# Kernel tuning notes

Hardware: AMD Instinct MI355X
Metric: run time of the kernel (lower is better)

The kernel has to match this reference:

```python
import jax, jax.numpy as jnp
import numpy as np

K1, K2, K3 = 36, 36, 2  # rolled-patch sizes hardcoded in unfolding()


def _patch_indices(C, H, W, k1=K1, k2=K2, k3=K3):
    """Precompute gather indices replacing the triple-nested torch.roll loops.

    Column col=(k*k2+j)*k1+i of Ak_3D holds X rolled by (k,i,j) along (C,H,W):
      A[b, c*H*W+h*W+w, col] = X[b, (c-k)%C, (h-i)%H, (w-j)%W]
    The adjoint gathers with +k,+i,+j shifts.
    """
    Kc = k1 * k2 * k3
    col = np.arange(Kc)
    kk = col // (k1 * k2)
    jj = (col % (k1 * k2)) // k1
    ii = col % k1
    cg, hg, wg = np.meshgrid(np.arange(C), np.arange(H), np.arange(W), indexing='ij')
    cg = cg.reshape(-1, 1); hg = hg.reshape(-1, 1); wg = wg.reshape(-1, 1)
    fwd = ((cg - kk) % C) * (H * W) + ((hg - ii) % H) * W + ((wg - jj) % W)
    adj = ((cg + kk) % C) * (H * W) + ((hg + ii) % H) * W + ((wg + jj) % W)
    return jnp.asarray(fwd, jnp.int32), jnp.asarray(adj, jnp.int32)


def _unfold(input_img, S0, alpha, beta, gamma, iters):
    B, C, H, W = input_img.shape
    m = C * H * W
    mk = (H * W) // 64
    Kc = K1 * K2 * K3
    fwd_idx, adj_idx = _patch_indices(C, H, W)
    colr = jnp.arange(Kc, dtype=jnp.int32)

    def Ak(x):  # [B,C,H,W] -> [B, m, Kc] (single gather == Ak_3D)
        return x.reshape(B, m)[:, fwd_idx]

    def Ak_adj(A):  # [B, m, Kc] -> [B,C,H,W] (== Ak_adj_3D)
        g = A[:, adj_idx, colr[None, :]]  # [B, m, Kc]
        return (g.sum(-1) / Kc).reshape(B, C, H, W)

    a3 = alpha[:, None, None]
    g3 = gamma[:, None, None]
    g4 = gamma[:, None, None, None]
    b4 = beta[:, None, None, None]
    I_mk = jnp.eye(mk, dtype=input_img.dtype)

    # t == 0 initialization (L detached, S random-clamped from setup, M/N rect. identities)
    L0 = jax.lax.stop_gradient(input_img)
    M0 = jnp.broadcast_to(jnp.eye(m, mk, dtype=input_img.dtype), (B, m, mk))
    N0 = jnp.broadcast_to(jnp.eye(mk, Kc, dtype=input_img.dtype), (B, mk, Kc))

    def step(carry, _):
        Lc, Sc, Mc, Nc = carry
        MN = Mc @ Nc                                        # [B, m, Kc]
        Ln = jnp.clip((input_img - Sc + g4 * Ak_adj(MN)) / (g4 + 1.0), 0.0, 1.0)
        Sn = (input_img - Ln) / (b4 + 1.0)
        AkL = Ak(Ln)                                        # [B, m, Kc]
        # M-update: 2g * Ak_L N^T pinv(a I + 2g N N^T)
        Cm = a3 * I_mk + 2.0 * g3 * (Nc @ Nc.transpose(0, 2, 1))      # [B, mk, mk]
        Mn = 2.0 * g3 * ((AkL @ Nc.transpose(0, 2, 1)) @ jnp.linalg.pinv(Cm))
        # N-update: 2g * pinv(a I + 2g M^T M) M^T Ak_L
        Cn = a3 * I_mk + 2.0 * g3 * (Mn.transpose(0, 2, 1) @ Mn)      # [B, mk, mk]
        Nn = 2.0 * g3 * (jnp.linalg.pinv(Cn) @ (Mn.transpose(0, 2, 1) @ AkL))
        return (Ln, Sn, Mn, Nn), None

    (Lf, _, _, _), _ = jax.lax.scan(step, (L0, S0, M0, N0), None, length=iters - 1)
    return Lf


def setup_inputs() -> dict:
    key = jax.random.key(0)
    k1, k2 = jax.random.split(key)
    B, C, H, W = 1, 2, 64, 64
    input_img = jax.random.uniform(k1, (B, C, H, W), jnp.float32)
    S0 = jnp.clip(jax.random.normal(k2, (B, C, H, W), jnp.float32), 0.0, 1.0)  # clamp(randn_like,0,1)
    alpha = jnp.full((B,), 10.0, jnp.float32)  # w_alpha
    beta = jnp.full((B,), 2.0, jnp.float32)    # w_beta
    gamma = jnp.full((B,), 10.0, jnp.float32)  # w_gamma
    return {"input_img": input_img, "S0": S0, "alpha": alpha, "beta": beta,
            "gamma": gamma, "iters": 6}


def reference(input_img, S0, alpha, beta, gamma, iters):
    return _unfold(input_img, S0, alpha, beta, gamma, iters)
```

## Files before the change

kernel.cpp:

```cpp
#include <hip/hip_runtime.h>

#define KC 2592
#define KCP 2624
#define HW 4096

#define OFF_L    0u
#define OFF_S    8192u
#define OFF_MT   16384u
#define OFF_NTT  540672u
#define OFF_BIG  708608u
#define OFF_GRAM 2805760u
#define OFF_CMI  2809856u
#define OFF_CNI  2813952u

__global__ __launch_bounds__(256) void k_init(const float* __restrict__ inp, const float* __restrict__ s0,
                                              float* __restrict__ L, float* __restrict__ S,
                                              float* __restrict__ Mt, float* __restrict__ NtT){
  int t = blockIdx.x * 256 + threadIdx.x;
  if (t < 8192){ L[t] = inp[t]; S[t] = s0[t]; }
  if (t < 524288){ int r = t >> 13; int p = t & 8191; Mt[t] = (p == r) ? 1.0f : 0.0f; }
  if (t < 167936){ int r = t / KCP; int d = t - r * KCP;
                   int dr = (r % 36) * 36 + r / 36;
                   NtT[t] = (d == dr) ? 1.0f : 0.0f; }
}

__device__ __forceinline__ float readlane_f(float x, int lane){
  return __uint_as_float(__builtin_amdgcn_readlane(__float_as_uint(x), lane));
}
template<int K>
__device__ __forceinline__ void gj_step(float (&b)[64], int lane){
  float bk = b[K];
  float akk = readlane_f(bk, K);
  float p = 1.0f / akk;
  bool isk = (lane == K);
  float t = isk ? 1.0f : bk;
  float pt = p * t;
  #pragma unroll
  for (int i = 0; i < 64; i++){
    if (i == K) continue;
    float f = readlane_f(b[i], K);
    float base = isk ? 0.0f : b[i];
    b[i] = fmaf(-f, pt, base);
  }
  b[K] = t * p;
}
template<int K> struct GJ {
  static __device__ __forceinline__ void run(float (&b)[64], int lane){
    gj_step<K>(b, lane);
    GJ<K + 1>::run(b, lane);
  }
};
template<> struct GJ<64> {
  static __device__ __forceinline__ void run(float (&b)[64], int lane){}
};
__device__ void inv64(const float* __restrict__ src, const float* __restrict__ pg,
                      const float* __restrict__ pa, float* __restrict__ dst, int lane){
  float scale = 2.0f * pg[0];
  float ad = pa[0];
  float b[64];
  #pragma unroll
  for (int i = 0; i < 64; i++)
    b[i] = scale * src[i * 64 + lane] + ((i == lane) ? ad : 0.0f);
  GJ<0>::run(b, lane);
  #pragma unroll
  for (int i = 0; i < 64; i++)
    dst[i * 64 + lane] = b[i];
}

__global__ __launch_bounds__(128) void k_conv_R(const float* __restrict__ Mtg,
                                                const float* __restrict__ NtT,
                                                float* __restrict__ Rpart){
  __shared__ float img[2][24][68];
  __shared__ float4 filt4[162];
  int r = blockIdx.x, oct = blockIdx.y, z = blockIdx.z, tid = threadIdx.x;
  int rowbase = oct * 16 + z * 9;
  const float4* gi4 = (const float4*)(Mtg + (size_t)r * 8192);
  for (int t = tid; t < 768; t += 128){
    int fw = t & 15, rr = t >> 4;
    int c = (rr >= 24) ? 1 : 0, q = rr - c * 24;
    int gr = (rowbase + q) & 63;
    float4 v4 = gi4[(c * 64 + gr) * 16 + fw];
    float* d = &img[c][q][fw * 4];
    d[0] = v4.x; d[1] = v4.y; d[2] = v4.z; d[3] = v4.w;
  }
  int iilo = z * 9;
  const float* gf = NtT + (size_t)r * KCP;
  for (int t = tid; t < 162; t += 128){
    int kk = t / 81; int rem4 = t - kk * 81;
    filt4[t] = *(const float4*)(gf + kk * 1296 + iilo * 36 + rem4 * 4);
  }
  __syncthreads();
  int c0 = tid >> 6, hl = (tid >> 2) & 15, w0 = (tid & 3) * 16;
  float acc[16];
  #pragma unroll
  for (int u = 0; u < 16; u++) acc[u] = 0.0f;
  #pragma unroll 1
  for (int kk = 0; kk < 2; kk++){
    int cimg = (c0 + kk) & 1;
    #pragma unroll 1
    for (int iix = 0; iix < 9; iix++){
      const float* ib = img[cimg][hl + iix];
      float v[32];
      #pragma unroll
      for (int t = 0; t < 8; t++){
        float4 t4 = *(const float4*)&ib[(w0 + 4 * t) & 63];
        v[4*t] = t4.x; v[4*t+1] = t4.y; v[4*t+2] = t4.z; v[4*t+3] = t4.w;
      }
      const float4* fb = &filt4[kk * 81 + iix * 9];
      #pragma unroll
      for (int g = 0; g < 9; g++){
        float4 ff = fb[g];
        #pragma unroll
        for (int u = 0; u < 16; u++) acc[u] = fmaf(ff.x, v[(4*g + 0 + u) & 31], acc[u]);
        #pragma unroll
        for (int u = 0; u < 16; u++) acc[u] = fmaf(ff.y, v[(4*g + 1 + u) & 31], acc[u]);
        #pragma unroll
        for (int u = 0; u < 16; u++) acc[u] = fmaf(ff.z, v[(4*g + 2 + u) & 31], acc[u]);
        #pragma unroll
        for (int u = 0; u < 16; u++) acc[u] = fmaf(ff.w, v[(4*g + 3 + u) & 31], acc[u]);
        if (g < 5){
          float4 nv = *(const float4*)&ib[(w0 + 32 + 4*g) & 63];
          int s = (4*g) & 31;
          v[s] = nv.x; v[s+1] = nv.y; v[s+2] = nv.z; v[s+3] = nv.w;
        }
      }
    }
  }
  int h = oct * 16 + hl;
  size_t ob = ((size_t)r + 64 * z) * 8192 + (size_t)(c0 * HW + h * 64 + w0);
  *(float4*)&Rpart[ob]      = make_float4(acc[0], acc[1], acc[2], acc[3]);
  *(float4*)&Rpart[ob + 4]  = make_float4(acc[4], acc[5], acc[6], acc[7]);
  *(float4*)&Rpart[ob + 8]  = make_float4(acc[8], acc[9], acc[10], acc[11]);
  *(float4*)&Rpart[ob + 12] = make_float4(acc[12], acc[13], acc[14], acc[15]);
}

__global__ __launch_bounds__(128) void k_conv_T1(const float* __restrict__ Lg,
                                                 const float* __restrict__ NtT,
                                                 float* __restrict__ T1t,
                                                 const float* __restrict__ Gr,
                                                 const float* __restrict__ pg,
                                                 const float* __restrict__ pa,
                                                 float* __restrict__ CmI){
  __shared__ float img[2][24][68];
  __shared__ float4 filt4[162];
  if (blockIdx.z == 4){
    if (blockIdx.x == 0 && blockIdx.y == 0 && threadIdx.x < 64)
      inv64(Gr, pg, pa, CmI, threadIdx.x);
    return;
  }
  int r = blockIdx.x, oct = blockIdx.y, z = blockIdx.z, tid = threadIdx.x;
  int rowbase = (oct * 16 - z * 9 - 8 + 128) & 63;
  const float4* gi4 = (const float4*)Lg;
  for (int t = tid; t < 768; t += 128){
    int fw = t & 15, rr = t >> 4;
    int c = (rr >= 24) ? 1 : 0, q = rr - c * 24;
    int gr = (rowbase + q) & 63;
    float4 v4 = gi4[(c * 64 + gr) * 16 + fw];
    float* d = &img[c][q][fw * 4];
    d[0] = v4.x; d[1] = v4.y; d[2] = v4.z; d[3] = v4.w;
  }
  int iilo = z * 9;
  const float* gf = NtT + (size_t)r * KCP;
  for (int t = tid; t < 162; t += 128){
    int kk = t / 81; int rem4 = t - kk * 81;
    filt4[t] = *(const float4*)(gf + kk * 1296 + iilo * 36 + rem4 * 4);
  }
  __syncthreads();
  int c0 = tid >> 6, hl = (tid >> 2) & 15, w0 = (tid & 3) * 16;
  float acc[16];
  #pragma unroll
  for (int u = 0; u < 16; u++) acc[u] = 0.0f;
  #pragma unroll 1
  for (int kk = 0; kk < 2; kk++){
    int cimg = (c0 - kk + 2) & 1;
    #pragma unroll 1
    for (int iix = 0; iix < 9; iix++){
      const float* ib = img[cimg][hl - iix + 8];
      float v[32];
      {
        float4 tm = *(const float4*)&ib[(w0 - 4 + 64) & 63];
        v[28] = tm.x; v[29] = tm.y; v[30] = tm.z; v[31] = tm.w;
      }
      #pragma unroll
      for (int t = 0; t < 4; t++){
        float4 t4 = *(const float4*)&ib[(w0 + 4 * t) & 63];
        v[4*t] = t4.x; v[4*t+1] = t4.y; v[4*t+2] = t4.z; v[4*t+3] = t4.w;
      }
      const float4* fb = &filt4[kk * 81 + iix * 9];
      #pragma unroll
      for (int g = 0; g < 9; g++){
        float4 ff = fb[g];
        #pragma unroll
        for (int u = 0; u < 16; u++) acc[u] = fmaf(ff.x, v[(u - (4*g + 0)) & 31], acc[u]);
        #pragma unroll
        for (int u = 0; u < 16; u++) acc[u] = fmaf(ff.y, v[(u - (4*g + 1)) & 31], acc[u]);
        #pragma unroll
        for (int u = 0; u < 16; u++) acc[u] = fmaf(ff.z, v[(u - (4*g + 2)) & 31], acc[u]);
        #pragma unroll
        for (int u = 0; u < 16; u++) acc[u] = fmaf(ff.w, v[(u - (4*g + 3)) & 31], acc[u]);
        if (g < 8){
          float4 nv = *(const float4*)&ib[(w0 - 8 - 4*g + 128) & 63];
          int s = (-8 - 4*g) & 31;
          v[s] = nv.x; v[s+1] = nv.y; v[s+2] = nv.z; v[s+3] = nv.w;
        }
      }
    }
  }
  int h = oct * 16 + hl;
  size_t ob = ((size_t)r + 64 * z) * 8192 + (size_t)(c0 * HW + h * 64 + w0);
  *(float4*)&T1t[ob]      = make_float4(acc[0], acc[1], acc[2], acc[3]);
  *(float4*)&T1t[ob + 4]  = make_float4(acc[4], acc[5], acc[6], acc[7]);
  *(float4*)&T1t[ob + 8]  = make_float4(acc[8], acc[9], acc[10], acc[11]);
  *(float4*)&T1t[ob + 12] = make_float4(acc[12], acc[13], acc[14], acc[15]);
}

__global__ __launch_bounds__(256) void k_reduce_LS(const float* __restrict__ Rpart,
                                                   const float* __restrict__ inp,
                                                   const float* __restrict__ pg, const float* __restrict__ pb,
                                                   float* __restrict__ S, float* __restrict__ Ldst){
  __shared__ float red[8][32];
  int tid = threadIdx.x;
  int pi = tid & 31, sg = tid >> 5;
  int p = blockIdx.x * 32 + pi;
  float acc = 0.0f;
  #pragma unroll 4
  for (int s = sg * 32; s < sg * 32 + 32; s++) acc += Rpart[(size_t)s * 8192 + p];
  red[sg][pi] = acc;
  __syncthreads();
  if (tid < 32){
    float a = 0.0f;
    #pragma unroll
    for (int q = 0; q < 8; q++) a += red[q][pi];
    float R = a * (1.0f / 2592.0f);
    float g = pg[0], b = pb[0];
    float Ln = (inp[p] - S[p] + g * R) / (g + 1.0f);
    Ln = fminf(fmaxf(Ln, 0.0f), 1.0f);
    S[p] = (inp[p] - Ln) / (b + 1.0f);
    Ldst[p] = Ln;
  }
}

__global__ __launch_bounds__(64) void k_gram(const float* __restrict__ rows, int stride, int len4,
                                             float* __restrict__ out){
  int e = blockIdx.x; int r1 = e >> 6, r2 = e & 63;
  if (r2 < r1) return;
  int lane = threadIdx.x;
  const float4* a = (const float4*)(rows + (size_t)r1 * stride);
  const float4* b = (const float4*)(rows + (size_t)r2 * stride);
  float acc = 0.0f;
  for (int p = lane; p < len4; p += 64){
    float4 x = a[p], y = b[p];
    acc = fmaf(x.x, y.x, acc); acc = fmaf(x.y, y.y, acc);
    acc = fmaf(x.z, y.z, acc); acc = fmaf(x.w, y.w, acc);
  }
  for (int off = 32; off; off >>= 1) acc += __shfl_down(acc, off, 64);
  if (lane == 0){ out[r1 * 64 + r2] = acc; out[r2 * 64 + r1] = acc; }
}

__global__ __launch_bounds__(256) void k_mn(const float* __restrict__ T1t, const float* __restrict__ CmInv,
                                            const float* __restrict__ pg, float* __restrict__ Mt){
  __shared__ float4 ci4[1024];
  int tid = threadIdx.x;
  const float4* g4 = (const float4*)CmInv;
  for (int t = tid; t < 1024; t += 256) ci4[t] = g4[t];
  __syncthreads();
  int p = blockIdx.x * 256 + tid;
  int sbase = blockIdx.y * 32;
  float g2 = 2.0f * pg[0];
  float acc[32];
  #pragma unroll
  for (int s = 0; s < 32; s++) acc[s] = 0.0f;
  for (int r = 0; r < 64; r++){
    float v = T1t[(size_t)r * 8192 + p] + T1t[(size_t)(r + 64) * 8192 + p]
            + T1t[(size_t)(r + 128) * 8192 + p] + T1t[(size_t)(r + 192) * 8192 + p];
    #pragma unroll
    for (int k = 0; k < 8; k++){
      float4 c = ci4[r * 16 + (sbase >> 2) + k];
      acc[4*k+0] = fmaf(v, c.x, acc[4*k+0]);
      acc[4*k+1] = fmaf(v, c.y, acc[4*k+1]);
      acc[4*k+2] = fmaf(v, c.z, acc[4*k+2]);
      acc[4*k+3] = fmaf(v, c.w, acc[4*k+3]);
    }
  }
  #pragma unroll
  for (int s = 0; s < 32; s++) Mt[(size_t)(sbase + s) * 8192 + p] = g2 * acc[s];
}

__global__ __launch_bounds__(256) void k_conv_T2(const float* __restrict__ Lg,
                                                 const float* __restrict__ Mtg,
                                                 float* __restrict__ T2part,
                                                 const float* __restrict__ Gr,
                                                 const float* __restrict__ pg,
                                                 const float* __restrict__ pa,
                                                 float* __restrict__ CnI){
  __shared__ float Mi[128 * 68];
  __shared__ float4 Ls4[256];
  if (blockIdx.y == 8){
    if (blockIdx.x == 0 && threadIdx.x < 64)
      inv64(Gr, pg, pa, CnI, threadIdx.x);
    return;
  }
  int r = blockIdx.x, hc = blockIdx.y, tid = threadIdx.x;
  const float4* gm4 = (const float4*)(Mtg + (size_t)r * 8192);
  for (int t = tid; t < 2048; t += 256){
    float4 v4 = gm4[t];
    int row = t >> 4, cb = (t & 15) * 4;
    float* d = &Mi[row * 68 + cb];
    d[0] = v4.x; d[1] = v4.y; d[2] = v4.z; d[3] = v4.w;
  }
  const float4* gl4 = (const float4*)Lg;
  if (tid < 256){
    int c = tid >> 7, rem = tid & 127;
    Ls4[tid] = gl4[c * 1024 + hc * 128 + rem];
  }
  __syncthreads();
  if (tid >= 216) return;
  int kk = tid / 108, rest = tid % 108, ii = rest / 3, jj0 = (rest % 3) * 12;
  float acc[12];
  #pragma unroll
  for (int u = 0; u < 12; u++) acc[u] = 0.0f;
  #pragma unroll 1
  for (int c = 0; c < 2; c++){
    #pragma unroll 1
    for (int hl = 0; hl < 8; hl++){
      int h = hc * 8 + hl;
      const float* ib = &Mi[(((c + kk) & 1) * 64 + ((h + ii) & 63)) * 68];
      const float4* lrow = &Ls4[c * 128 + hl * 16];
      float v[16];
      {
        float4 t0 = *(const float4*)&ib[jj0];
        float4 t1 = *(const float4*)&ib[jj0 + 4];
        float4 t2 = *(const float4*)&ib[jj0 + 8];
        float4 t3 = *(const float4*)&ib[jj0 + 12];
        v[0]=t0.x; v[1]=t0.y; v[2]=t0.z; v[3]=t0.w;
        v[4]=t1.x; v[5]=t1.y; v[6]=t1.z; v[7]=t1.w;
        v[8]=t2.x; v[9]=t2.y; v[10]=t2.z; v[11]=t2.w;
        v[12]=t3.x; v[13]=t3.y; v[14]=t3.z; v[15]=t3.w;
      }
      #pragma unroll
      for (int wg = 0; wg < 16; wg++){
        float4 lv = lrow[wg];
        #pragma unroll
        for (int u = 0; u < 12; u++) acc[u] = fmaf(lv.x, v[(4*wg + 0 + u) & 15], acc[u]);
        #pragma unroll
        for (int u = 0; u < 12; u++) acc[u] = fmaf(lv.y, v[(4*wg + 1 + u) & 15], acc[u]);
        #pragma unroll
        for (int u = 0; u < 12; u++) acc[u] = fmaf(lv.z, v[(4*wg + 2 + u) & 15], acc[u]);
        #pragma unroll
        for (int u = 0; u < 12; u++) acc[u] = fmaf(lv.w, v[(4*wg + 3 + u) & 15], acc[u]);
        if (wg < 15){
          float4 nv = *(const float4*)&ib[(jj0 + 4*wg + 16) & 63];
          int s = (4*wg) & 15;
          v[s] = nv.x; v[s+1] = nv.y; v[s+2] = nv.z; v[s+3] = nv.w;
        }
      }
    }
  }
  #pragma unroll
  for (int u = 0; u < 12; u++){
    int col = kk * 1296 + (jj0 + u) * 36 + ii;
    T2part[((size_t)hc * 64 + r) * KC + col] = acc[u];
  }
}

__global__ __launch_bounds__(256) void k_t2sum(const float* __restrict__ T2part, float* __restrict__ T2sum){
  int t = blockIdx.x * 256 + threadIdx.x;
  float s = 0.0f;
  #pragma unroll
  for (int hc = 0; hc < 8; hc++) s += T2part[(size_t)hc * 165888 + t];
  T2sum[t] = s;
}

__global__ __launch_bounds__(256) void k_nn(const float* __restrict__ T2sum, const float* __restrict__ CnInv,
                                            const float* __restrict__ pg,
                                            float* __restrict__ NtT){
  __shared__ float4 ci4[1024];
  int tid = threadIdx.x;
  const float4* g4 = (const float4*)CnInv;
  for (int t = tid; t < 1024; t += 256) ci4[t] = g4[t];
  __syncthreads();
  int col = blockIdx.x * 256 + tid;
  if (col >= KC) return;
  int rb = blockIdx.y * 16;
  float g2 = 2.0f * pg[0];
  float acc[16];
  #pragma unroll
  for (int rr = 0; rr < 16; rr++) acc[rr] = 0.0f;
  for (int s = 0; s < 64; s++){
    float tv = T2sum[(size_t)s * KC + col];
    #pragma unroll
    for (int k = 0; k < 4; k++){
      float4 c = ci4[s * 16 + (rb >> 2) + k];
      acc[4*k+0] = fmaf(tv, c.x, acc[4*k+0]);
      acc[4*k+1] = fmaf(tv, c.y, acc[4*k+1]);
      acc[4*k+2] = fmaf(tv, c.z, acc[4*k+2]);
      acc[4*k+3] = fmaf(tv, c.w, acc[4*k+3]);
    }
  }
  int kk = col / 1296, rest = col % 1296, jj = rest / 36, iv = rest % 36;
  int d = (kk * 36 + iv) * 36 + jj;
  #pragma unroll
  for (int rr = 0; rr < 16; rr++){
    NtT[(size_t)(rb + rr) * KCP + d] = g2 * acc[rr];
  }
}

extern "C" void kernel_launch(void* const* d_in, const int* in_sizes, int n_in,
                              void* d_out, int out_size, void* d_ws, size_t ws_size,
                              hipStream_t stream) {
  const float* inp = (const float*)d_in[0];
  const float* s0  = (const float*)d_in[1];
  const float* pa  = (const float*)d_in[2];
  const float* pb  = (const float*)d_in[3];
  const float* pg  = (const float*)d_in[4];
  float* ws  = (float*)d_ws;
  float* L   = ws + OFF_L;   float* S   = ws + OFF_S;    float* Mt  = ws + OFF_MT;
  float* NtT = ws + OFF_NTT; float* Big = ws + OFF_BIG;
  float* T2p = ws + OFF_BIG;
  float* T2s = ws + OFF_BIG + 1327104u;
  float* Gr  = ws + OFF_GRAM;
  float* CmI = ws + OFF_CMI; float* CnI = ws + OFF_CNI;
  float* out = (float*)d_out;

  k_init<<<2048, 256, 0, stream>>>(inp, s0, L, S, Mt, NtT);
  for (int step = 0; step < 5; step++){
    k_conv_R<<<dim3(64, 4, 4), 128, 0, stream>>>(Mt, NtT, Big);
    bool last = (step == 4);
    k_reduce_LS<<<256, 256, 0, stream>>>(Big, inp, pg, pb, S, last ? out : L);
    if (last) break;
    k_gram<<<4096, 64, 0, stream>>>(NtT, KCP, KCP / 4, Gr);
    k_conv_T1<<<dim3(64, 4, 5), 128, 0, stream>>>(L, NtT, Big, Gr, pg, pa, CmI);
    k_mn<<<dim3(32, 2), 256, 0, stream>>>(Big, CmI, pg, Mt);
    k_gram<<<4096, 64, 0, stream>>>(Mt, 8192, 2048, Gr);
    k_conv_T2<<<dim3(64, 9), 256, 0, stream>>>(L, Mt, T2p, Gr, pg, pa, CnI);
    k_t2sum<<<648, 256, 0, stream>>>(T2p, T2s);
    k_nn<<<dim3(11, 4), 256, 0, stream>>>(T2s, CnI, pg, NtT);
  }
}
```

Measured before the change: 987.6 us.

## Move Cm inverse into conv_R launch and use LDS multi-warp Gauss-Jordan

After: 1.599 ms. 61.9% more time.

```diff
diff --git a/kernel.cpp b/kernel.cpp
--- a/kernel.cpp
+++ b/kernel.cpp
@@ -24,54 +24,61 @@
                    NtT[t] = (d == dr) ? 1.0f : 0.0f; }
 }
 
-__device__ __forceinline__ float readlane_f(float x, int lane){
-  return __uint_as_float(__builtin_amdgcn_readlane(__float_as_uint(x), lane));
-}
-template<int K>
-__device__ __forceinline__ void gj_step(float (&b)[64], int lane){
-  float bk = b[K];
-  float akk = readlane_f(bk, K);
-  float p = 1.0f / akk;
-  bool isk = (lane == K);
-  float t = isk ? 1.0f : bk;
-  float pt = p * t;
-  #pragma unroll
-  for (int i = 0; i < 64; i++){
-    if (i == K) continue;
-    float f = readlane_f(b[i], K);
-    float base = isk ? 0.0f : b[i];
-    b[i] = fmaf(-f, pt, base);
-  }
-  b[K] = t * p;
-}
-template<int K> struct GJ {
-  static __device__ __forceinline__ void run(float (&b)[64], int lane){
-    gj_step<K>(b, lane);
-    GJ<K + 1>::run(b, lane);
-  }
-};
-template<> struct GJ<64> {
-  static __device__ __forceinline__ void run(float (&b)[64], int lane){}
-};
-__device__ void inv64(const float* __restrict__ src, const float* __restrict__ pg,
-                      const float* __restrict__ pa, float* __restrict__ dst, int lane){
-  float scale = 2.0f * pg[0];
-  float ad = pa[0];
-  float b[64];
-  #pragma unroll
-  for (int i = 0; i < 64; i++)
-    b[i] = scale * src[i * 64 + lane] + ((i == lane) ? ad : 0.0f);
-  GJ<0>::run(b, lane);
-  #pragma unroll
-  for (int i = 0; i < 64; i++)
-    dst[i * 64 + lane] = b[i];
+template<int NT>
+__device__ void inv64_lds(const float* __restrict__ src, const float* __restrict__ pg,
+                          const float* __restrict__ pa, float* __restrict__ dst,
+                          int tid, float* __restrict__ A, float* __restrict__ rowj,
+                          float* __restrict__ colj){
+  const int ROWS = 64 / (NT / 64);
+  float scale = 2.0f * pg[0], ad = pa[0];
+  for (int t = tid; t < 4096; t += NT){
+    int i = t >> 6, c = t & 63;
+    A[i * 65 + c] = scale * src[t] + ((i == c) ? ad : 0.0f);
+  }
+  __syncthreads();
+  int c = tid & 63, q = tid >> 6;
+  int i0 = q * ROWS;
+  #pragma unroll 1
+  for (int j = 0; j < 64; j++){
+    if (tid < 64) rowj[tid] = A[j * 65 + tid];
+    else if (tid < 128) colj[tid - 64] = A[(tid - 64) * 65 + j];
+    __syncthreads();
+    float p = 1.0f / rowj[j];
+    float rc = rowj[c];
+    bool cj = (c == j);
+    float rcp = rc * p;
+    #pragma unroll
+    for (int r = 0; r < ROWS; r++){
+      int i = i0 + r;
+      float old = A[i * 65 + c];
+      float fi = colj[i];
+      float nonpiv = cj ? (-fi * p) : fmaf(-fi, rcp, old);
+      float pivrow = cj ? p : rcp;
+      A[i * 65 + c] = (i == j) ? pivrow : nonpiv;
+    }
+    __syncthreads();
+  }
+  for (int t = tid; t < 4096; t += NT)
+    dst[t] = A[(t >> 6) * 65 + (t & 63)];
 }
 
 __global__ __launch_bounds__(128) void k_conv_R(const float* __restrict__ Mtg,
                                                 const float* __restrict__ NtT,
-                                                float* __restrict__ Rpart){
+                                                float* __restrict__ Rpart,
+                                                const float* __restrict__ Gr,
+                                                const float* __restrict__ pg,
+                                                const float* __restrict__ pa,
+                                                float* __restrict__ CmI){
   __shared__ float img[2][24][68];
   __shared__ float4 filt4[162];
+  __shared__ float Ai[64 * 65];
+  __shared__ float rowj[64];
+  __shared__ float colj[64];
+  if (blockIdx.z == 4){
+    if (blockIdx.x == 0 && blockIdx.y == 0)
+      inv64_lds<128>(Gr, pg, pa, CmI, threadIdx.x, Ai, rowj, colj);
+    return;
+  }
   int r = blockIdx.x, oct = blockIdx.y, z = blockIdx.z, tid = threadIdx.x;
   int rowbase = oct * 16 + z * 9;
   const float4* gi4 = (const float4*)(Mtg + (size_t)r * 8192);
@@ -136,18 +143,9 @@
 
 __global__ __launch_bounds__(128) void k_conv_T1(const float* __restrict__ Lg,
                                                  const float* __restrict__ NtT,
-                                                 float* __restrict__ T1t,
-                                                 const float* __restrict__ Gr,
-                                                 const float* __restrict__ pg,
-                                                 const float* __restrict__ pa,
-                                                 float* __restrict__ CmI){
+                                                 float* __restrict__ T1t){
   __shared__ float img[2][24][68];
   __shared__ float4 filt4[162];
-  if (blockIdx.z == 4){
-    if (blockIdx.x == 0 && blockIdx.y == 0 && threadIdx.x < 64)
-      inv64(Gr, pg, pa, CmI, threadIdx.x);
-    return;
-  }
   int r = blockIdx.x, oct = blockIdx.y, z = blockIdx.z, tid = threadIdx.x;
   int rowbase = (oct * 16 - z * 9 - 8 + 128) & 63;
   const float4* gi4 = (const float4*)Lg;
@@ -295,9 +293,12 @@
                                                  float* __restrict__ CnI){
   __shared__ float Mi[128 * 68];
   __shared__ float4 Ls4[256];
+  __shared__ float Ai[64 * 65];
+  __shared__ float rowj[64];
+  __shared__ float colj[64];
   if (blockIdx.y == 8){
-    if (blockIdx.x == 0 && threadIdx.x < 64)
-      inv64(Gr, pg, pa, CnI, threadIdx.x);
+    if (blockIdx.x == 0)
+      inv64_lds<256>(Gr, pg, pa, CnI, threadIdx.x, Ai, rowj, colj);
     return;
   }
   int r = blockIdx.x, hc = blockIdx.y, tid = threadIdx.x;
@@ -424,12 +425,13 @@
 
   k_init<<<2048, 256, 0, stream>>>(inp, s0, L, S, Mt, NtT);
   for (int step = 0; step < 5; step++){
-    k_conv_R<<<dim3(64, 4, 4), 128, 0, stream>>>(Mt, NtT, Big);
     bool last = (step == 4);
+    if (!last)
+      k_gram<<<4096, 64, 0, stream>>>(NtT, KCP, KCP / 4, Gr);
+    k_conv_R<<<dim3(64, 4, last ? 4 : 5), 128, 0, stream>>>(Mt, NtT, Big, Gr, pg, pa, CmI);
     k_reduce_LS<<<256, 256, 0, stream>>>(Big, inp, pg, pb, S, last ? out : L);
     if (last) break;
-    k_gram<<<4096, 64, 0, stream>>>(NtT, KCP, KCP / 4, Gr);
-    k_conv_T1<<<dim3(64, 4, 5), 128, 0, stream>>>(L, NtT, Big, Gr, pg, pa, CmI);
+    k_conv_T1<<<dim3(64, 4, 4), 128, 0, stream>>>(L, NtT, Big);
     k_mn<<<dim3(32, 2), 256, 0, stream>>>(Big, CmI, pg, Mt);
     k_gram<<<4096, 64, 0, stream>>>(Mt, 8192, 2048, Gr);
     k_conv_T2<<<dim3(64, 9), 256, 0, stream>>>(L, Mt, T2p, Gr, pg, pa, CnI);
```
